# Performance work log

Hardware: AMD Instinct MI355X
Metric: run time of the kernel (lower is better)

The kernel has to match this reference:

```python
import jax, jax.numpy as jnp
import numpy as np

T, B, C = 2048, 8, 1024
H, K, P = 16, 31, 15  # num_heads, kernel_size, padding_l
R = C // H


def setup_inputs() -> dict:
    key = jax.random.key(0)
    k1, k2 = jax.random.split(key)
    x = jax.random.normal(k1, (T, B, C), dtype=jnp.float32)
    # weight_linear.weight, xavier-ish scale, shape (H*K, C)
    W = jax.random.normal(k2, (H * K, C), dtype=jnp.float32) * (2.0 / (C + H * K)) ** 0.5
    return {"x": x, "W": W}


def reference(x, W):
    # per-position dynamic kernels: (T,B,H,K)
    w = jnp.einsum('tbc,oc->tbo', x, W).reshape(T, B, H, K)
    w = jax.nn.softmax(w, axis=-1)  # weight_softmax=True
    # depthwise dynamic conv: out[t] = sum_k w[t,:,:,k] * x[t - P + k]
    xr = x.reshape(T, B, H, R)
    xp = jnp.pad(xr, ((P, K - 1 - P), (0, 0), (0, 0), (0, 0)))
    out = jnp.zeros_like(xr)
    for k in range(K):  # fixed small kernel-size loop, fuses under jit
        out = out + w[:, :, :, k:k + 1] * jax.lax.dynamic_slice_in_dim(xp, k, T, axis=0)
    return out.reshape(T, B, C)
```

## Files before the change

### kernel.cpp

```cpp
#include <hip/hip_runtime.h>
#include <cstddef>
#include <cstdint>

constexpr int T_ = 2048;
constexpr int B_ = 8;
constexpr int C_ = 1024;
constexpr int H_ = 16;
constexpr int K_ = 31;
constexpr int P_ = 15;
constexpr int M_ = T_ * B_;
constexpr int N_ = H_ * K_;
constexpr int NP = 512;

typedef _Float16 f16x4 __attribute__((ext_vector_type(4)));
typedef _Float16 f16x8 __attribute__((ext_vector_type(8)));
typedef float f32x4 __attribute__((ext_vector_type(4)));

__device__ __forceinline__ void async_cp16(const void* g, void* l) {
    __builtin_amdgcn_global_load_lds(
        (const __attribute__((address_space(1))) void*)g,
        (__attribute__((address_space(3))) void*)l, 16, 0, 0);
}

constexpr int XCH = M_ * C_ / 8;
constexpr int WCH = NP * C_ / 8;

__global__ __launch_bounds__(256)
void cvt_inputs(const float* __restrict__ X, const float* __restrict__ W,
                _Float16* __restrict__ Xh, _Float16* __restrict__ Wh) {
    const int id = blockIdx.x * 256 + threadIdx.x;
    if (id < XCH) {
        const float4 v0 = *(const float4*)(X + (size_t)id * 8);
        const float4 v1 = *(const float4*)(X + (size_t)id * 8 + 4);
        f16x8 hv;
        hv[0] = (_Float16)v0.x; hv[1] = (_Float16)v0.y;
        hv[2] = (_Float16)v0.z; hv[3] = (_Float16)v0.w;
        hv[4] = (_Float16)v1.x; hv[5] = (_Float16)v1.y;
        hv[6] = (_Float16)v1.z; hv[7] = (_Float16)v1.w;
        *(f16x8*)(Xh + (size_t)id * 8) = hv;
    } else {
        const int j = id - XCH;
        const int n = j >> 7, sp = j & 127;
        const int h = n >> 5, k = n & 31;
        f16x8 hv = {};
        if (k < 31) {
            const float* wp = W + (size_t)(h * 31 + k) * C_ + sp * 8;
            const float4 v0 = *(const float4*)(wp);
            const float4 v1 = *(const float4*)(wp + 4);
            hv[0] = (_Float16)v0.x; hv[1] = (_Float16)v0.y;
            hv[2] = (_Float16)v0.z; hv[3] = (_Float16)v0.w;
            hv[4] = (_Float16)v1.x; hv[5] = (_Float16)v1.y;
            hv[6] = (_Float16)v1.z; hv[7] = (_Float16)v1.w;
        }
        *(f16x8*)(Wh + (size_t)n * C_ + sp * 8) = hv;
    }
}

__global__ __launch_bounds__(256)
void gemm_softmax(const _Float16* __restrict__ Xh,
                  const _Float16* __restrict__ Wh,
                  _Float16* __restrict__ WSM) {
    __shared__ union {
        struct { _Float16 A[3][128 * 64]; _Float16 B[2][128 * 64]; } s;
        _Float16 Ls[128 * 136];
    } u;

    const int tid = threadIdx.x;
    const int lane = tid & 63;
    const int w = tid >> 6;
    const int wm = (w >> 1) * 64;
    const int wn = (w & 1) * 64;
    const int col = lane & 15;
    const int g = lane >> 4;
    const int m0 = blockIdx.x * 128;
    const int n0 = blockIdx.y * 128;

    const _Float16* asrc[4];
    const _Float16* bsrc[4];
#pragma unroll
    for (int p = 0; p < 4; ++p) {
        const int ci = p * 256 + tid;
        const int r = ci >> 3, cs = ci & 7;
        const int cl = cs ^ (r & 7);
        asrc[p] = Xh + (size_t)(m0 + r) * C_ + cl * 8;
        bsrc[p] = Wh + (size_t)(n0 + r) * C_ + cl * 8;
    }

    f32x4 acc[4][4] = {};

#pragma unroll
    for (int p = 0; p < 4; ++p) {
        const int ci = p * 256 + tid;
        async_cp16(asrc[p], &u.s.A[0][ci * 8]);
    }
#pragma unroll
    for (int p = 0; p < 4; ++p) {
        const int ci = p * 256 + tid;
        async_cp16(bsrc[p], &u.s.B[0][ci * 8]);
    }
#pragma unroll
    for (int p = 0; p < 4; ++p) {
        const int ci = p * 256 + tid;
        async_cp16(asrc[p] + 64, &u.s.A[1][ci * 8]);
    }
    asm volatile("s_waitcnt vmcnt(4)" ::: "memory");
    __builtin_amdgcn_s_barrier();
    __builtin_amdgcn_sched_barrier(0);

    for (int t = 0; t < 16; ++t) {
        const int ca = t % 3, cb = t & 1;
        if (t < 15) {
            const int k1 = (t + 1) * 64;
#pragma unroll
            for (int p = 0; p < 4; ++p) {
                const int ci = p * 256 + tid;
                async_cp16(bsrc[p] + k1, &u.s.B[cb ^ 1][ci * 8]);
            }
        }
        if (t < 14) {
            const int k2 = (t + 2) * 64;
            const int ca2 = (t + 2) % 3;
#pragma unroll
            for (int p = 0; p < 4; ++p) {
                const int ci = p * 256 + tid;
                async_cp16(asrc[p] + k2, &u.s.A[ca2][ci * 8]);
            }
        }

        f16x8 a[2][4], b[2][4];
#pragma unroll
        for (int kk = 0; kk < 2; ++kk) {
#pragma unroll
            for (int mf = 0; mf < 4; ++mf) {
                const int row = wm + mf * 16 + col;
                const int c = ((kk << 2) | g) ^ (row & 7);
                a[kk][mf] = *(const f16x8*)&u.s.A[ca][row * 64 + c * 8];
            }
#pragma unroll
            for (int nf = 0; nf < 4; ++nf) {
                const int row = wn + nf * 16 + col;
                const int c = ((kk << 2) | g) ^ (row & 7);
                b[kk][nf] = *(const f16x8*)&u.s.B[cb][row * 64 + c * 8];
            }
        }
#pragma unroll
        for (int kk = 0; kk < 2; ++kk)
#pragma unroll
            for (int nf = 0; nf < 4; ++nf)
#pragma unroll
                for (int mf = 0; mf < 4; ++mf)
                    acc[mf][nf] = __builtin_amdgcn_mfma_f32_16x16x32_f16(
                        a[kk][mf], b[kk][nf], acc[mf][nf], 0, 0, 0);

        if (t < 14) {
            asm volatile("s_waitcnt vmcnt(4)" ::: "memory");
        } else {
            asm volatile("s_waitcnt vmcnt(0)" ::: "memory");
        }
        __builtin_amdgcn_s_barrier();
        __builtin_amdgcn_sched_barrier(0);
    }

    const int rb = g * 4;
#pragma unroll
    for (int nf = 0; nf < 4; ++nf) {
        const int nl = wn + nf * 16 + col;
#pragma unroll
        for (int mf = 0; mf < 4; ++mf) {
            const int row = wm + mf * 16 + rb;
#pragma unroll
            for (int r = 0; r < 4; ++r)
                u.Ls[(row + r) * 136 + nl] = (_Float16)acc[mf][nf][r];
        }
    }
    __syncthreads();

#pragma unroll
    for (int p = 0; p < 2; ++p) {
        const int task = tid + p * 256;
        const int row = task >> 2, hl = task & 3;
        const _Float16* lp = &u.Ls[row * 136 + hl * 32];
        float v[32];
#pragma unroll
        for (int c = 0; c < 4; ++c) {
            const f16x8 ch = *(const f16x8*)(lp + c * 8);
#pragma unroll
            for (int e = 0; e < 8; ++e) v[c * 8 + e] = (float)ch[e];
        }
        float mx = v[0];
#pragma unroll
        for (int k = 1; k < 31; ++k) mx = fmaxf(mx, v[k]);
        float ssum = 0.f;
#pragma unroll
        for (int k = 0; k < 31; ++k) { v[k] = __expf(v[k] - mx); ssum += v[k]; }
        const float inv = 1.f / ssum;
        _Float16* op = WSM + (size_t)(m0 + row) * NP + n0 + hl * 32;
#pragma unroll
        for (int c = 0; c < 4; ++c) {
            f16x8 ov;
#pragma unroll
            for (int e = 0; e < 8; ++e) {
                const int k = c * 8 + e;
                ov[e] = (k < 31) ? (_Float16)(v[k] * inv) : (_Float16)0.f;
            }
            *(f16x8*)(op + c * 8) = ov;
        }
    }
}

__global__ __launch_bounds__(256)
void dconv(const _Float16* __restrict__ Xh, const _Float16* __restrict__ WSM,
           float* __restrict__ out) {
    __shared__ float xs[94][64];
    __shared__ float ws[64][36];

    const int tid = threadIdx.x;
    const int t0 = blockIdx.x * 64;
    const int bh = (int)blockIdx.y;
    const int b = bh >> 4, h = bh & 15;

    for (int task = tid; task < 94 * 8; task += 256) {
        const int r = task >> 3, hc = task & 7;
        const int tp = t0 + r - 15;
        f16x8 v = {};
        if (tp >= 0 && tp < T_)
            v = *(const f16x8*)(Xh + ((size_t)tp * B_ + b) * C_ + h * 64 + hc * 8);
        f32x4 lo, hi;
        lo[0] = (float)v[0]; lo[1] = (float)v[1];
        lo[2] = (float)v[2]; lo[3] = (float)v[3];
        hi[0] = (float)v[4]; hi[1] = (float)v[5];
        hi[2] = (float)v[6]; hi[3] = (float)v[7];
        const int c0 = (2 * hc) ^ (r & 7), c1 = (2 * hc + 1) ^ (r & 7);
        *(f32x4*)&xs[r][c0 * 4] = lo;
        *(f32x4*)&xs[r][c1 * 4] = hi;
    }
    {
        const int t = tid >> 2, kc = (tid & 3) * 8;
        const f16x8 wv =
            *(const f16x8*)(WSM + ((size_t)(t0 + t) * B_ + b) * NP + h * 32 + kc);
        f32x4 lo, hi;
        lo[0] = (float)wv[0]; lo[1] = (float)wv[1];
        lo[2] = (float)wv[2]; lo[3] = (float)wv[3];
        hi[0] = (float)wv[4]; hi[1] = (float)wv[5];
        hi[2] = (float)wv[6]; hi[3] = (float)wv[7];
        *(f32x4*)&ws[t][kc] = lo;
        *(f32x4*)&ws[t][kc + 4] = hi;
    }
    __syncthreads();

    const int s = tid & 15;
    const int tg4 = (tid >> 4) * 4;
    f32x4 acc[4] = {};
    f32x4 wc[4];

#pragma unroll
    for (int rr = 0; rr < 34; ++rr) {
        const int r = tg4 + rr;
        const f32x4 xv = *(const f32x4*)&xs[r][(s ^ (r & 7)) * 4];
#pragma unroll
        for (int i = 0; i < 4; ++i) {
            const int k = rr - i;
            if (k < 0 || k > 30) continue;
            if ((k & 3) == 0) wc[i] = *(const f32x4*)&ws[tg4 + i][k];
            acc[i] += wc[i][k & 3] * xv;
        }
    }

#pragma unroll
    for (int i = 0; i < 4; ++i) {
        const int t = t0 + tg4 + i;
        *(f32x4*)(out + ((size_t)t * B_ + b) * C_ + h * 64 + s * 4) = acc[i];
    }
}

extern "C" void kernel_launch(void* const* d_in, const int* in_sizes, int n_in,
                              void* d_out, int out_size, void* d_ws,
                              size_t ws_size, hipStream_t stream) {
    const float* X = (const float*)d_in[0];
    const float* W = (const float*)d_in[1];
    float* out = (float*)d_out;

    _Float16* Wh = (_Float16*)d_ws;
    _Float16* WSM = (_Float16*)((char*)d_ws + (size_t)NP * C_ * 2);
    _Float16* Xh = (_Float16*)((char*)d_ws + (size_t)NP * C_ * 2 +
                               (size_t)M_ * NP * 2);

    cvt_inputs<<<(XCH + WCH) / 256, 256, 0, stream>>>(X, W, Xh, Wh);
    gemm_softmax<<<dim3(M_ / 128, NP / 128), 256, 0, stream>>>(Xh, Wh, WSM);
    dconv<<<dim3(T_ / 64, B_ * H_), 256, 0, stream>>>(Xh, WSM, out);
}
```

Baseline: 73.69 us.

## Fuse GEMM-softmax with dynamic convolution, keeping softmax weights in LDS

Merges the GEMM+softmax kernel and the depthwise dynamic conv kernel into one kernel. Each block's softmax weights for 16 timesteps × 8 batches × 4 heads stay in shared memory and are consumed directly by a conv loop over 8 head/batch-half iterations. This removes the WSM global write and read and one kernel launch. In exchange, every block reloads a 46-row halo of x per iteration, which adds redundant global traffic. Shared memory grows to 80KB, which may lower occupancy.

```diff
diff --git a/kernel.cpp b/kernel.cpp
--- a/kernel.cpp
+++ b/kernel.cpp
@@ -57,13 +57,14 @@
 }
 
 __global__ __launch_bounds__(256)
-void gemm_softmax(const _Float16* __restrict__ Xh,
-                  const _Float16* __restrict__ Wh,
-                  _Float16* __restrict__ WSM) {
-    __shared__ union {
-        struct { _Float16 A[3][128 * 64]; _Float16 B[2][128 * 64]; } s;
-        _Float16 Ls[128 * 136];
-    } u;
+void fused_gsc(const _Float16* __restrict__ Xh, const _Float16* __restrict__ Wh,
+               float* __restrict__ out) {
+    __shared__ __align__(16) char smem[81920];
+    _Float16* const As = (_Float16*)smem;
+    _Float16* const Bs = (_Float16*)(smem + 49152);
+    _Float16* const Ls = (_Float16*)smem;
+    _Float16* const Wls = (_Float16*)(smem + 49152);
+    float (* const xs)[64] = (float(*)[64])smem;
 
     const int tid = threadIdx.x;
     const int lane = tid & 63;
@@ -91,17 +92,17 @@
 #pragma unroll
     for (int p = 0; p < 4; ++p) {
         const int ci = p * 256 + tid;
-        async_cp16(asrc[p], &u.s.A[0][ci * 8]);
-    }
-#pragma unroll
-    for (int p = 0; p < 4; ++p) {
-        const int ci = p * 256 + tid;
-        async_cp16(bsrc[p], &u.s.B[0][ci * 8]);
-    }
-#pragma unroll
-    for (int p = 0; p < 4; ++p) {
-        const int ci = p * 256 + tid;
-        async_cp16(asrc[p] + 64, &u.s.A[1][ci * 8]);
+        async_cp16(asrc[p], As + ci * 8);
+    }
+#pragma unroll
+    for (int p = 0; p < 4; ++p) {
+        const int ci = p * 256 + tid;
+        async_cp16(bsrc[p], Bs + ci * 8);
+    }
+#pragma unroll
+    for (int p = 0; p < 4; ++p) {
+        const int ci = p * 256 + tid;
+        async_cp16(asrc[p] + 64, As + 8192 + ci * 8);
     }
     asm volatile("s_waitcnt vmcnt(4)" ::: "memory");
     __builtin_amdgcn_s_barrier();
@@ -114,7 +115,7 @@
 #pragma unroll
             for (int p = 0; p < 4; ++p) {
                 const int ci = p * 256 + tid;
-                async_cp16(bsrc[p] + k1, &u.s.B[cb ^ 1][ci * 8]);
+                async_cp16(bsrc[p] + k1, Bs + (cb ^ 1) * 8192 + ci * 8);
             }
         }
         if (t < 14) {
@@ -123,7 +124,7 @@
 #pragma unroll
             for (int p = 0; p < 4; ++p) {
                 const int ci = p * 256 + tid;
-                async_cp16(asrc[p] + k2, &u.s.A[ca2][ci * 8]);
+                async_cp16(asrc[p] + k2, As + ca2 * 8192 + ci * 8);
             }
         }
 
@@ -134,13 +135,13 @@
             for (int mf = 0; mf < 4; ++mf) {
                 const int row = wm + mf * 16 + col;
                 const int c = ((kk << 2) | g) ^ (row & 7);
-                a[kk][mf] = *(const f16x8*)&u.s.A[ca][row * 64 + c * 8];
+                a[kk][mf] = *(const f16x8*)&As[ca * 8192 + row * 64 + c * 8];
             }
 #pragma unroll
             for (int nf = 0; nf < 4; ++nf) {
                 const int row = wn + nf * 16 + col;
                 const int c = ((kk << 2) | g) ^ (row & 7);
-                b[kk][nf] = *(const f16x8*)&u.s.B[cb][row * 64 + c * 8];
+                b[kk][nf] = *(const f16x8*)&Bs[cb * 8192 + row * 64 + c * 8];
             }
         }
 #pragma unroll
@@ -170,7 +171,7 @@
             const int row = wm + mf * 16 + rb;
 #pragma unroll
             for (int r = 0; r < 4; ++r)
-                u.Ls[(row + r) * 136 + nl] = (_Float16)acc[mf][nf][r];
+                Ls[(row + r) * 136 + nl] = (_Float16)acc[mf][nf][r];
         }
     }
     __syncthreads();
@@ -179,7 +180,7 @@
     for (int p = 0; p < 2; ++p) {
         const int task = tid + p * 256;
         const int row = task >> 2, hl = task & 3;
-        const _Float16* lp = &u.Ls[row * 136 + hl * 32];
+        const _Float16* lp = &Ls[row * 136 + hl * 32];
         float v[32];
 #pragma unroll
         for (int c = 0; c < 4; ++c) {
@@ -194,7 +195,7 @@
 #pragma unroll
         for (int k = 0; k < 31; ++k) { v[k] = __expf(v[k] - mx); ssum += v[k]; }
         const float inv = 1.f / ssum;
-        _Float16* op = WSM + (size_t)(m0 + row) * NP + n0 + hl * 32;
+        _Float16* op = &Wls[(hl * 128 + row) * 32];
 #pragma unroll
         for (int c = 0; c < 4; ++c) {
             f16x8 ov;
@@ -206,70 +207,64 @@
             *(f16x8*)(op + c * 8) = ov;
         }
     }
-}
-
-__global__ __launch_bounds__(256)
-void dconv(const _Float16* __restrict__ Xh, const _Float16* __restrict__ WSM,
-           float* __restrict__ out) {
-    __shared__ float xs[94][64];
-    __shared__ float ws[64][36];
-
-    const int tid = threadIdx.x;
-    const int t0 = blockIdx.x * 64;
-    const int bh = (int)blockIdx.y;
-    const int b = bh >> 4, h = bh & 15;
-
-    for (int task = tid; task < 94 * 8; task += 256) {
-        const int r = task >> 3, hc = task & 7;
-        const int tp = t0 + r - 15;
-        f16x8 v = {};
-        if (tp >= 0 && tp < T_)
-            v = *(const f16x8*)(Xh + ((size_t)tp * B_ + b) * C_ + h * 64 + hc * 8);
-        f32x4 lo, hi;
-        lo[0] = (float)v[0]; lo[1] = (float)v[1];
-        lo[2] = (float)v[2]; lo[3] = (float)v[3];
-        hi[0] = (float)v[4]; hi[1] = (float)v[5];
-        hi[2] = (float)v[6]; hi[3] = (float)v[7];
-        const int c0 = (2 * hc) ^ (r & 7), c1 = (2 * hc + 1) ^ (r & 7);
-        *(f32x4*)&xs[r][c0 * 4] = lo;
-        *(f32x4*)&xs[r][c1 * 4] = hi;
-    }
-    {
-        const int t = tid >> 2, kc = (tid & 3) * 8;
-        const f16x8 wv =
-            *(const f16x8*)(WSM + ((size_t)(t0 + t) * B_ + b) * NP + h * 32 + kc);
-        f32x4 lo, hi;
-        lo[0] = (float)wv[0]; lo[1] = (float)wv[1];
-        lo[2] = (float)wv[2]; lo[3] = (float)wv[3];
-        hi[0] = (float)wv[4]; hi[1] = (float)wv[5];
-        hi[2] = (float)wv[6]; hi[3] = (float)wv[7];
-        *(f32x4*)&ws[t][kc] = lo;
-        *(f32x4*)&ws[t][kc + 4] = hi;
-    }
-    __syncthreads();
-
+
+    const int t0 = blockIdx.x * 16;
+    const int hbase = blockIdx.y * 4;
     const int s = tid & 15;
-    const int tg4 = (tid >> 4) * 4;
-    f32x4 acc[4] = {};
-    f32x4 wc[4];
-
-#pragma unroll
-    for (int rr = 0; rr < 34; ++rr) {
-        const int r = tg4 + rr;
-        const f32x4 xv = *(const f32x4*)&xs[r][(s ^ (r & 7)) * 4];
+    const int grp = tid >> 4;
+    const int bl = grp & 3;
+    const int tquad = (grp >> 2) * 4;
+
+    for (int iter = 0; iter < 8; ++iter) {
+        const int hl = iter >> 1, bh = iter & 1;
+        const int h = hbase + hl;
+        __syncthreads();
+
+        for (int task = tid; task < 184 * 8; task += 256) {
+            const int r184 = task >> 3, hc = task & 7;
+            const int r46 = r184 >> 2, bb = r184 & 3;
+            const int t = t0 + r46 - 15;
+            f16x8 v = {};
+            if (t >= 0 && t < T_)
+                v = *(const f16x8*)(Xh + (size_t)(t * 8 + bh * 4 + bb) * C_ +
+                                    h * 64 + hc * 8);
+            f32x4 lo, hi;
+            lo[0] = (float)v[0]; lo[1] = (float)v[1];
+            lo[2] = (float)v[2]; lo[3] = (float)v[3];
+            hi[0] = (float)v[4]; hi[1] = (float)v[5];
+            hi[2] = (float)v[6]; hi[3] = (float)v[7];
+            const int sw = r184 & 7;
+            *(f32x4*)&xs[r184][((2 * hc) ^ sw) * 4] = lo;
+            *(f32x4*)&xs[r184][((2 * hc + 1) ^ sw) * 4] = hi;
+        }
+        __syncthreads();
+
+        const int bglob = bh * 4 + bl;
+        f32x4 cacc[4] = {};
+        f32x4 wc[4];
+#pragma unroll
+        for (int rr = 0; rr < 34; ++rr) {
+            const int r184 = (tquad + rr) * 4 + bl;
+            const f32x4 xv = *(const f32x4*)&xs[r184][(s ^ (r184 & 7)) * 4];
+#pragma unroll
+            for (int i = 0; i < 4; ++i) {
+                const int k = rr - i;
+                if (k < 0 || k > 30) continue;
+                if ((k & 3) == 0) {
+                    const f16x4 wq = *(const f16x4*)
+                        &Wls[(hl * 128 + (tquad + i) * 8 + bglob) * 32 + k];
+                    wc[i][0] = (float)wq[0]; wc[i][1] = (float)wq[1];
+                    wc[i][2] = (float)wq[2]; wc[i][3] = (float)wq[3];
+                }
+                cacc[i] += wc[i][k & 3] * xv;
+            }
+        }
 #pragma unroll
         for (int i = 0; i < 4; ++i) {
-            const int k = rr - i;
-            if (k < 0 || k > 30) continue;
-            if ((k & 3) == 0) wc[i] = *(const f32x4*)&ws[tg4 + i][k];
-            acc[i] += wc[i][k & 3] * xv;
-        }
-    }
-
-#pragma unroll
-    for (int i = 0; i < 4; ++i) {
-        const int t = t0 + tg4 + i;
-        *(f32x4*)(out + ((size_t)t * B_ + b) * C_ + h * 64 + s * 4) = acc[i];
+            const int t = t0 + tquad + i;
+            *(f32x4*)(out + (size_t)(t * 8 + bglob) * C_ + h * 64 + s * 4) =
+                cacc[i];
+        }
     }
 }
 
@@ -281,11 +276,8 @@
     float* out = (float*)d_out;
 
     _Float16* Wh = (_Float16*)d_ws;
-    _Float16* WSM = (_Float16*)((char*)d_ws + (size_t)NP * C_ * 2);
-    _Float16* Xh = (_Float16*)((char*)d_ws + (size_t)NP * C_ * 2 +
-                               (size_t)M_ * NP * 2);
+    _Float16* Xh = (_Float16*)((char*)d_ws + (size_t)NP * C_ * 2);
 
     cvt_inputs<<<(XCH + WCH) / 256, 256, 0, stream>>>(X, W, Xh, Wh);
-    gemm_softmax<<<dim3(M_ / 128, NP / 128), 256, 0, stream>>>(Xh, Wh, WSM);
-    dconv<<<dim3(T_ / 64, B_ * H_), 256, 0, stream>>>(Xh, WSM, out);
-}
+    fused_gsc<<<dim3(M_ / 128, NP / 128), 256, 0, stream>>>(Xh, Wh, out);
+}
```

Result: slower. 76.13 us (+3.3%).

## Fuse X fp32-to-fp16 conversion into GEMM A-tile loads, read fp32 X in dconv

Applied to the files above, without the earlier changes.

Drops the separate conversion pass over X. The GEMM now loads fp32 A tiles into registers, converts them and writes them into a double-buffered LDS tile, while B moves to triple-buffered async copies. The dconv kernel reads fp32 X directly, which also gives it the exact fp32 values. This removes a full write and re-read of a half-precision copy of X. The cost is that A loads are no longer async-to-LDS, and each of the 4 N-blocks now reads fp32 X itself, doubling A-side traffic and adding register pressure and a convert step inside the GEMM loop.

```diff
diff --git a/kernel.cpp b/kernel.cpp
--- a/kernel.cpp
+++ b/kernel.cpp
@@ -22,46 +22,29 @@
         (__attribute__((address_space(3))) void*)l, 16, 0, 0);
 }
 
-constexpr int XCH = M_ * C_ / 8;
-constexpr int WCH = NP * C_ / 8;
-
 __global__ __launch_bounds__(256)
-void cvt_inputs(const float* __restrict__ X, const float* __restrict__ W,
-                _Float16* __restrict__ Xh, _Float16* __restrict__ Wh) {
-    const int id = blockIdx.x * 256 + threadIdx.x;
-    if (id < XCH) {
-        const float4 v0 = *(const float4*)(X + (size_t)id * 8);
-        const float4 v1 = *(const float4*)(X + (size_t)id * 8 + 4);
-        f16x8 hv;
+void cvt_w(const float* __restrict__ W, _Float16* __restrict__ Wh) {
+    const int j = blockIdx.x * 256 + threadIdx.x;
+    const int n = j >> 7, sp = j & 127;
+    const int h = n >> 5, k = n & 31;
+    f16x8 hv = {};
+    if (k < 31) {
+        const float* wp = W + (size_t)(h * 31 + k) * C_ + sp * 8;
+        const float4 v0 = *(const float4*)(wp);
+        const float4 v1 = *(const float4*)(wp + 4);
         hv[0] = (_Float16)v0.x; hv[1] = (_Float16)v0.y;
         hv[2] = (_Float16)v0.z; hv[3] = (_Float16)v0.w;
         hv[4] = (_Float16)v1.x; hv[5] = (_Float16)v1.y;
         hv[6] = (_Float16)v1.z; hv[7] = (_Float16)v1.w;
-        *(f16x8*)(Xh + (size_t)id * 8) = hv;
-    } else {
-        const int j = id - XCH;
-        const int n = j >> 7, sp = j & 127;
-        const int h = n >> 5, k = n & 31;
-        f16x8 hv = {};
-        if (k < 31) {
-            const float* wp = W + (size_t)(h * 31 + k) * C_ + sp * 8;
-            const float4 v0 = *(const float4*)(wp);
-            const float4 v1 = *(const float4*)(wp + 4);
-            hv[0] = (_Float16)v0.x; hv[1] = (_Float16)v0.y;
-            hv[2] = (_Float16)v0.z; hv[3] = (_Float16)v0.w;
-            hv[4] = (_Float16)v1.x; hv[5] = (_Float16)v1.y;
-            hv[6] = (_Float16)v1.z; hv[7] = (_Float16)v1.w;
-        }
-        *(f16x8*)(Wh + (size_t)n * C_ + sp * 8) = hv;
-    }
+    }
+    *(f16x8*)(Wh + (size_t)n * C_ + sp * 8) = hv;
 }
 
 __global__ __launch_bounds__(256)
-void gemm_softmax(const _Float16* __restrict__ Xh,
-                  const _Float16* __restrict__ Wh,
+void gemm_softmax(const float* __restrict__ X, const _Float16* __restrict__ Wh,
                   _Float16* __restrict__ WSM) {
     __shared__ union {
-        struct { _Float16 A[3][128 * 64]; _Float16 B[2][128 * 64]; } s;
+        struct { _Float16 A[2][128 * 64]; _Float16 B[3][128 * 64]; } s;
         _Float16 Ls[128 * 136];
     } u;
 
@@ -75,57 +58,60 @@
     const int m0 = blockIdx.x * 128;
     const int n0 = blockIdx.y * 128;
 
-    const _Float16* asrc[4];
+    const int ar = tid >> 1;
+    const int acs0 = (tid & 1) * 4;
+    const float* axbase = X + (size_t)(m0 + ar) * C_;
+
     const _Float16* bsrc[4];
 #pragma unroll
     for (int p = 0; p < 4; ++p) {
         const int ci = p * 256 + tid;
         const int r = ci >> 3, cs = ci & 7;
         const int cl = cs ^ (r & 7);
-        asrc[p] = Xh + (size_t)(m0 + r) * C_ + cl * 8;
         bsrc[p] = Wh + (size_t)(n0 + r) * C_ + cl * 8;
     }
 
     f32x4 acc[4][4] = {};
-
-#pragma unroll
-    for (int p = 0; p < 4; ++p) {
-        const int ci = p * 256 + tid;
-        async_cp16(asrc[p], &u.s.A[0][ci * 8]);
-    }
-#pragma unroll
-    for (int p = 0; p < 4; ++p) {
-        const int ci = p * 256 + tid;
-        async_cp16(bsrc[p], &u.s.B[0][ci * 8]);
-    }
-#pragma unroll
-    for (int p = 0; p < 4; ++p) {
-        const int ci = p * 256 + tid;
-        async_cp16(asrc[p] + 64, &u.s.A[1][ci * 8]);
-    }
-    asm volatile("s_waitcnt vmcnt(4)" ::: "memory");
+    float4 areg[4][2];
+
+#define LOAD_A(k0)                                                        \
+    _Pragma("unroll")                                                     \
+    for (int q = 0; q < 4; ++q) {                                         \
+        const int cl = (acs0 + q) ^ (ar & 7);                             \
+        const float* src = axbase + (k0) + cl * 8;                        \
+        areg[q][0] = *(const float4*)src;                                 \
+        areg[q][1] = *(const float4*)(src + 4);                           \
+    }
+#define WRITE_A(buf)                                                      \
+    _Pragma("unroll")                                                     \
+    for (int q = 0; q < 4; ++q) {                                         \
+        f16x8 hv;                                                         \
+        hv[0] = (_Float16)areg[q][0].x; hv[1] = (_Float16)areg[q][0].y;   \
+        hv[2] = (_Float16)areg[q][0].z; hv[3] = (_Float16)areg[q][0].w;   \
+        hv[4] = (_Float16)areg[q][1].x; hv[5] = (_Float16)areg[q][1].y;   \
+        hv[6] = (_Float16)areg[q][1].z; hv[7] = (_Float16)areg[q][1].w;   \
+        *(f16x8*)&u.s.A[buf][ar * 64 + (acs0 + q) * 8] = hv;              \
+    }
+#define ISSUE_B(k0, buf)                                                  \
+    _Pragma("unroll")                                                     \
+    for (int p = 0; p < 4; ++p) {                                         \
+        const int ci = p * 256 + tid;                                     \
+        async_cp16(bsrc[p] + (k0), &u.s.B[buf][ci * 8]);                  \
+    }
+
+    LOAD_A(0);
+    ISSUE_B(0, 0);
+    ISSUE_B(64, 1);
+    asm volatile("s_waitcnt vmcnt(8)" ::: "memory");
+    WRITE_A(0);
+    asm volatile("s_waitcnt vmcnt(4) lgkmcnt(0)" ::: "memory");
     __builtin_amdgcn_s_barrier();
     __builtin_amdgcn_sched_barrier(0);
 
     for (int t = 0; t < 16; ++t) {
-        const int ca = t % 3, cb = t & 1;
-        if (t < 15) {
-            const int k1 = (t + 1) * 64;
-#pragma unroll
-            for (int p = 0; p < 4; ++p) {
-                const int ci = p * 256 + tid;
-                async_cp16(bsrc[p] + k1, &u.s.B[cb ^ 1][ci * 8]);
-            }
-        }
-        if (t < 14) {
-            const int k2 = (t + 2) * 64;
-            const int ca2 = (t + 2) % 3;
-#pragma unroll
-            for (int p = 0; p < 4; ++p) {
-                const int ci = p * 256 + tid;
-                async_cp16(asrc[p] + k2, &u.s.A[ca2][ci * 8]);
-            }
-        }
+        const int ca = t & 1, cb = t % 3;
+        if (t < 15) { LOAD_A((t + 1) * 64); }
+        if (t < 14) { ISSUE_B((t + 2) * 64, (t + 2) % 3); }
 
         f16x8 a[2][4], b[2][4];
 #pragma unroll
@@ -157,6 +143,8 @@
         } else {
             asm volatile("s_waitcnt vmcnt(0)" ::: "memory");
         }
+        if (t < 15) { WRITE_A(ca ^ 1); }
+        asm volatile("s_waitcnt lgkmcnt(0)" ::: "memory");
         __builtin_amdgcn_s_barrier();
         __builtin_amdgcn_sched_barrier(0);
     }
@@ -206,10 +194,13 @@
             *(f16x8*)(op + c * 8) = ov;
         }
     }
+#undef LOAD_A
+#undef WRITE_A
+#undef ISSUE_B
 }
 
 __global__ __launch_bounds__(256)
-void dconv(const _Float16* __restrict__ Xh, const _Float16* __restrict__ WSM,
+void dconv(const float* __restrict__ X, const _Float16* __restrict__ WSM,
            float* __restrict__ out) {
     __shared__ float xs[94][64];
     __shared__ float ws[64][36];
@@ -219,20 +210,13 @@
     const int bh = (int)blockIdx.y;
     const int b = bh >> 4, h = bh & 15;
 
-    for (int task = tid; task < 94 * 8; task += 256) {
-        const int r = task >> 3, hc = task & 7;
+    for (int task = tid; task < 94 * 16; task += 256) {
+        const int r = task >> 4, sc = task & 15;
         const int tp = t0 + r - 15;
-        f16x8 v = {};
+        f32x4 v = {};
         if (tp >= 0 && tp < T_)
-            v = *(const f16x8*)(Xh + ((size_t)tp * B_ + b) * C_ + h * 64 + hc * 8);
-        f32x4 lo, hi;
-        lo[0] = (float)v[0]; lo[1] = (float)v[1];
-        lo[2] = (float)v[2]; lo[3] = (float)v[3];
-        hi[0] = (float)v[4]; hi[1] = (float)v[5];
-        hi[2] = (float)v[6]; hi[3] = (float)v[7];
-        const int c0 = (2 * hc) ^ (r & 7), c1 = (2 * hc + 1) ^ (r & 7);
-        *(f32x4*)&xs[r][c0 * 4] = lo;
-        *(f32x4*)&xs[r][c1 * 4] = hi;
+            v = *(const f32x4*)(X + ((size_t)tp * B_ + b) * C_ + h * 64 + sc * 4);
+        *(f32x4*)&xs[r][(sc ^ (r & 7)) * 4] = v;
     }
     {
         const int t = tid >> 2, kc = (tid & 3) * 8;
@@ -282,10 +266,8 @@
 
     _Float16* Wh = (_Float16*)d_ws;
     _Float16* WSM = (_Float16*)((char*)d_ws + (size_t)NP * C_ * 2);
-    _Float16* Xh = (_Float16*)((char*)d_ws + (size_t)NP * C_ * 2 +
-                               (size_t)M_ * NP * 2);
-
-    cvt_inputs<<<(XCH + WCH) / 256, 256, 0, stream>>>(X, W, Xh, Wh);
-    gemm_softmax<<<dim3(M_ / 128, NP / 128), 256, 0, stream>>>(Xh, Wh, WSM);
-    dconv<<<dim3(T_ / 64, B_ * H_), 256, 0, stream>>>(Xh, WSM, out);
-}
+
+    cvt_w<<<256, 256, 0, stream>>>(W, Wh);
+    gemm_softmax<<<dim3(M_ / 128, NP / 128), 256, 0, stream>>>(X, Wh, WSM);
+    dconv<<<dim3(T_ / 64, B_ * H_), 256, 0, stream>>>(X, WSM, out);
+}
```

Result: slower. 90.77 us (+23.2%).

## Compute softmax in registers via cross-lane shuffles and raise MFMA priority

Applied to the files above, without the earlier changes.

Drops the LDS staging buffer and the extra barrier in the GEMM epilogue. Softmax over each head's 31 logits is now computed straight from the MFMA accumulators, using 16-lane xor shuffles for the max and the sum. It also wraps the MFMA block in s_setprio so math waves get issue priority. The trade-off is many shuffle ops and scattered 2-byte global stores in place of vectorized 16-byte stores.

```diff
diff --git a/kernel.cpp b/kernel.cpp
--- a/kernel.cpp
+++ b/kernel.cpp
@@ -60,10 +60,8 @@
 void gemm_softmax(const _Float16* __restrict__ Xh,
                   const _Float16* __restrict__ Wh,
                   _Float16* __restrict__ WSM) {
-    __shared__ union {
-        struct { _Float16 A[3][128 * 64]; _Float16 B[2][128 * 64]; } s;
-        _Float16 Ls[128 * 136];
-    } u;
+    __shared__ _Float16 As[3][128 * 64];
+    __shared__ _Float16 Bs[2][128 * 64];
 
     const int tid = threadIdx.x;
     const int lane = tid & 63;
@@ -91,17 +89,17 @@
 #pragma unroll
     for (int p = 0; p < 4; ++p) {
         const int ci = p * 256 + tid;
-        async_cp16(asrc[p], &u.s.A[0][ci * 8]);
-    }
-#pragma unroll
-    for (int p = 0; p < 4; ++p) {
-        const int ci = p * 256 + tid;
-        async_cp16(bsrc[p], &u.s.B[0][ci * 8]);
-    }
-#pragma unroll
-    for (int p = 0; p < 4; ++p) {
-        const int ci = p * 256 + tid;
-        async_cp16(asrc[p] + 64, &u.s.A[1][ci * 8]);
+        async_cp16(asrc[p], &As[0][ci * 8]);
+    }
+#pragma unroll
+    for (int p = 0; p < 4; ++p) {
+        const int ci = p * 256 + tid;
+        async_cp16(bsrc[p], &Bs[0][ci * 8]);
+    }
+#pragma unroll
+    for (int p = 0; p < 4; ++p) {
+        const int ci = p * 256 + tid;
+        async_cp16(asrc[p] + 64, &As[1][ci * 8]);
     }
     asm volatile("s_waitcnt vmcnt(4)" ::: "memory");
     __builtin_amdgcn_s_barrier();
@@ -114,7 +112,7 @@
 #pragma unroll
             for (int p = 0; p < 4; ++p) {
                 const int ci = p * 256 + tid;
-                async_cp16(bsrc[p] + k1, &u.s.B[cb ^ 1][ci * 8]);
+                async_cp16(bsrc[p] + k1, &Bs[cb ^ 1][ci * 8]);
             }
         }
         if (t < 14) {
@@ -123,7 +121,7 @@
 #pragma unroll
             for (int p = 0; p < 4; ++p) {
                 const int ci = p * 256 + tid;
-                async_cp16(asrc[p] + k2, &u.s.A[ca2][ci * 8]);
+                async_cp16(asrc[p] + k2, &As[ca2][ci * 8]);
             }
         }
 
@@ -134,15 +132,16 @@
             for (int mf = 0; mf < 4; ++mf) {
                 const int row = wm + mf * 16 + col;
                 const int c = ((kk << 2) | g) ^ (row & 7);
-                a[kk][mf] = *(const f16x8*)&u.s.A[ca][row * 64 + c * 8];
+                a[kk][mf] = *(const f16x8*)&As[ca][row * 64 + c * 8];
             }
 #pragma unroll
             for (int nf = 0; nf < 4; ++nf) {
                 const int row = wn + nf * 16 + col;
                 const int c = ((kk << 2) | g) ^ (row & 7);
-                b[kk][nf] = *(const f16x8*)&u.s.B[cb][row * 64 + c * 8];
-            }
-        }
+                b[kk][nf] = *(const f16x8*)&Bs[cb][row * 64 + c * 8];
+            }
+        }
+        __builtin_amdgcn_s_setprio(1);
 #pragma unroll
         for (int kk = 0; kk < 2; ++kk)
 #pragma unroll
@@ -151,6 +150,7 @@
                 for (int mf = 0; mf < 4; ++mf)
                     acc[mf][nf] = __builtin_amdgcn_mfma_f32_16x16x32_f16(
                         a[kk][mf], b[kk][nf], acc[mf][nf], 0, 0, 0);
+        __builtin_amdgcn_s_setprio(0);
 
         if (t < 14) {
             asm volatile("s_waitcnt vmcnt(4)" ::: "memory");
@@ -161,49 +161,43 @@
         __builtin_amdgcn_sched_barrier(0);
     }
 
-    const int rb = g * 4;
-#pragma unroll
-    for (int nf = 0; nf < 4; ++nf) {
-        const int nl = wn + nf * 16 + col;
-#pragma unroll
-        for (int mf = 0; mf < 4; ++mf) {
-            const int row = wm + mf * 16 + rb;
-#pragma unroll
-            for (int r = 0; r < 4; ++r)
-                u.Ls[(row + r) * 136 + nl] = (_Float16)acc[mf][nf][r];
-        }
-    }
-    __syncthreads();
-
-#pragma unroll
-    for (int p = 0; p < 2; ++p) {
-        const int task = tid + p * 256;
-        const int row = task >> 2, hl = task & 3;
-        const _Float16* lp = &u.Ls[row * 136 + hl * 32];
-        float v[32];
-#pragma unroll
-        for (int c = 0; c < 4; ++c) {
-            const f16x8 ch = *(const f16x8*)(lp + c * 8);
-#pragma unroll
-            for (int e = 0; e < 8; ++e) v[c * 8 + e] = (float)ch[e];
-        }
-        float mx = v[0];
-#pragma unroll
-        for (int k = 1; k < 31; ++k) mx = fmaxf(mx, v[k]);
-        float ssum = 0.f;
-#pragma unroll
-        for (int k = 0; k < 31; ++k) { v[k] = __expf(v[k] - mx); ssum += v[k]; }
-        const float inv = 1.f / ssum;
-        _Float16* op = WSM + (size_t)(m0 + row) * NP + n0 + hl * 32;
-#pragma unroll
-        for (int c = 0; c < 4; ++c) {
-            f16x8 ov;
-#pragma unroll
-            for (int e = 0; e < 8; ++e) {
-                const int k = c * 8 + e;
-                ov[e] = (k < 31) ? (_Float16)(v[k] * inv) : (_Float16)0.f;
-            }
-            *(f16x8*)(op + c * 8) = ov;
+    const bool tail = (col == 15);
+#pragma unroll
+    for (int mf = 0; mf < 4; ++mf) {
+#pragma unroll
+        for (int ri = 0; ri < 4; ++ri) {
+            const int row = wm + mf * 16 + g * 4 + ri;
+            const float v0 = acc[mf][0][ri];
+            const float v1 = acc[mf][1][ri];
+            const float v2 = acc[mf][2][ri];
+            const float v3 = acc[mf][3][ri];
+            const float u1 = tail ? -1e30f : v1;
+            const float u3 = tail ? -1e30f : v3;
+            float mA = fmaxf(v0, u1);
+            float mB = fmaxf(v2, u3);
+#pragma unroll
+            for (int d = 1; d < 16; d <<= 1) {
+                mA = fmaxf(mA, __shfl_xor(mA, d));
+                mB = fmaxf(mB, __shfl_xor(mB, d));
+            }
+            const float e0 = __expf(v0 - mA);
+            const float e1 = tail ? 0.f : __expf(v1 - mA);
+            const float e2 = __expf(v2 - mB);
+            const float e3 = tail ? 0.f : __expf(v3 - mB);
+            float sA = e0 + e1;
+            float sB = e2 + e3;
+#pragma unroll
+            for (int d = 1; d < 16; d <<= 1) {
+                sA += __shfl_xor(sA, d);
+                sB += __shfl_xor(sB, d);
+            }
+            const float iA = 1.f / sA;
+            const float iB = 1.f / sB;
+            _Float16* op = WSM + (size_t)(m0 + row) * NP + n0 + wn + col;
+            op[0]  = (_Float16)(e0 * iA);
+            op[16] = (_Float16)(e1 * iA);
+            op[32] = (_Float16)(e2 * iB);
+            op[48] = (_Float16)(e3 * iB);
         }
     }
 }
```

After: 76.02 us. 3.2% more time.
